# Kernel optimization log

Measured on AMD Instinct MI355X. Metric: run time of the kernel, lower is better.

Reference implementation:

```python
import jax, jax.numpy as jnp
import numpy as np

LOG_VAR_Q = 0.0
TEMPERATURE = 0.5


def setup_inputs() -> dict:
    key = jax.random.key(0)
    k1, k2, k3 = jax.random.split(key, 3)
    bs, dim_z, W, H, K = 64, 64, 32, 32, 1024
    x = jax.random.normal(k1, (bs, dim_z, W, H), dtype=jnp.float32)
    codebook = jax.random.normal(k2, (K, dim_z), dtype=jnp.float32)
    log_var_q_scalar = jnp.asarray(0.0, dtype=jnp.float32)
    # pre-sampled standard Gumbel noise for the relaxed categorical
    u = jax.random.uniform(k3, (bs * W * H, K), dtype=jnp.float32,
                           minval=1e-6, maxval=1.0 - 1e-6)
    gumbel_noise = -jnp.log(-jnp.log(u))
    return {"x": x, "codebook": codebook,
            "log_var_q_scalar": log_var_q_scalar,
            "gumbel_noise": gumbel_noise}


def reference(x, codebook, log_var_q_scalar, gumbel_noise):
    bs, dim_z, W, H = x.shape
    # [bs, dim_z, W, H] -> [bs*W*H, dim_z]
    x_flat = jnp.transpose(x, (0, 2, 3, 1)).reshape(-1, dim_z)

    var_q = jnp.exp(jnp.asarray(LOG_VAR_Q, x.dtype)) + jnp.exp(log_var_q_scalar)
    precision_q = 1.0 / jnp.clip(var_q, 1e-10)
    w = 0.5 * precision_q  # scalar weight on squared distances

    sq_x = jnp.sum(x_flat * x_flat, axis=-1, keepdims=True)
    sq_c = jnp.sum(codebook * codebook, axis=-1)
    cross = jnp.einsum('nd,kd->nk', x_flat, codebook)
    logit = -w * (sq_x - 2.0 * cross + sq_c)

    log_probs = jax.nn.log_softmax(logit, axis=-1)
    probs = jnp.exp(log_probs)

    # gumbel-softmax relaxed one-hot encodings
    encodings = jax.nn.softmax((logit + gumbel_noise) / TEMPERATURE, axis=-1)

    quantized = jnp.einsum('nk,kd->nd', encodings, codebook)
    quantized = jnp.transpose(quantized.reshape(bs, W, H, dim_z), (0, 3, 1, 2))

    kld_discrete = jnp.sum(probs * log_probs) / bs
    kld_continuous = jnp.mean(jnp.sum(w * (x - quantized) ** 2, axis=(1, 2, 3)))
    return quantized, kld_discrete + kld_continuous
```

## Files before the change

kernel.cpp:

```cpp
#include <hip/hip_runtime.h>
#include <math.h>

#define K_CB 1024
#define D_Z  64
#define MT   32
#define NTOT 65536
#define NBLK (NTOT / MT)

typedef __attribute__((ext_vector_type(8)))  short s16x8;
typedef __attribute__((ext_vector_type(4)))  short s16x4;
typedef __attribute__((ext_vector_type(4)))  float f32x4;
typedef __attribute__((ext_vector_type(16))) float f32x16;

#define WS_CB16  0
#define WS_CBT16 131072
#define WS_NWSQC 262144
#define WS_PART  266240

__device__ __forceinline__ unsigned short f2b(float f) {
  unsigned int u = __float_as_uint(f);
  u += 0x7fffu + ((u >> 16) & 1u);
  return (unsigned short)(u >> 16);
}

__global__ void vq_prep(const float* __restrict__ cb, const float* __restrict__ lvq,
                        unsigned char* __restrict__ wsb) {
  unsigned short* cb16  = (unsigned short*)(wsb + WS_CB16);
  unsigned short* cbT16 = (unsigned short*)(wsb + WS_CBT16);
  float* nwsqc = (float*)(wsb + WS_NWSQC);
  const float w = 0.5f / fmaxf(1.0f + __expf(lvq[0]), 1e-10f);
  const int tid = threadIdx.x;
  const int k  = blockIdx.x * 16 + (tid >> 4);
  const int d0 = (tid & 15) * 4;
  const f32x4 v = *(const f32x4*)(cb + k * D_Z + d0);
  s16x4 b4;
  #pragma unroll
  for (int i = 0; i < 4; i++) b4[i] = (short)f2b(v[i]);
  *(s16x4*)(cb16 + k * D_Z + d0) = b4;
  #pragma unroll
  for (int i = 0; i < 4; i++) cbT16[(d0 + i) * K_CB + k] = (unsigned short)b4[i];
  float s = v[0]*v[0] + v[1]*v[1] + v[2]*v[2] + v[3]*v[3];
  #pragma unroll
  for (int off = 1; off < 16; off <<= 1) s += __shfl_xor(s, off);
  if ((tid & 15) == 0) nwsqc[k] = -w * s;
}

__global__ __launch_bounds__(512, 4)
void vq_main(const float* __restrict__ x, const float* __restrict__ gum,
             const float* __restrict__ lvq, unsigned char* __restrict__ wsb,
             float* __restrict__ out) {
  __shared__ __align__(16) unsigned short xa[MT * D_Z];
  __shared__ __align__(16) unsigned short es[MT * K_CB];
  __shared__ __align__(16) float stats[8][MT][4];
  __shared__ __align__(16) float s2s[8][MT];
  __shared__ float kldrow[MT];
  __shared__ float wred[8];

  const int tid  = threadIdx.x;
  const int w    = tid >> 6;
  const int lane = tid & 63;
  const int m32  = lane & 31;
  const int hi   = lane >> 5;
  const int bid  = blockIdx.x;
  const int blk  = ((bid & 7) << 8) | (bid >> 3);
  const int row0 = blk * MT;
  const int bidx = row0 >> 10;
  const int rem0 = row0 & 1023;
  const int kw0  = w << 7;

  const float wq = 0.5f / fmaxf(1.0f + __expf(lvq[0]), 1e-10f);
  const float w2 = 2.0f * wq;

  const unsigned short* cb16  = (const unsigned short*)(wsb + WS_CB16);
  const unsigned short* cbT16 = (const unsigned short*)(wsb + WS_CBT16);
  const float* nwsqc = (const float*)(wsb + WS_NWSQC);

  {
    const int m = tid & 31, dg = tid >> 5;
    #pragma unroll
    for (int i = 0; i < 4; i++) {
      const int d = dg + 16 * i;
      const float v = x[((bidx * D_Z + d) << 10) + rem0 + m];
      xa[(m * D_Z + d) ^ ((m & 7) << 3)] = f2b(v);
    }
  }
  __syncthreads();

  f32x16 acc[4];
  #pragma unroll
  for (int t = 0; t < 4; t++)
    #pragma unroll
    for (int r = 0; r < 16; r++) acc[t][r] = 0.f;
  {
    s16x8 bx[4];
    #pragma unroll
    for (int kb = 0; kb < 4; kb++) {
      const int byteoff = (m32 * 128 + kb * 32 + hi * 16) ^ ((m32 & 7) << 4);
      bx[kb] = *(const s16x8*)((const unsigned char*)xa + byteoff);
    }
    #pragma unroll
    for (int t = 0; t < 4; t++) {
      const unsigned short* ap = cb16 + (kw0 + t * 32 + m32) * D_Z + hi * 8;
      #pragma unroll
      for (int kb = 0; kb < 4; kb++) {
        const s16x8 a = *(const s16x8*)(ap + kb * 16);
        acc[t] = __builtin_amdgcn_mfma_f32_32x32x16_bf16(a, bx[kb], acc[t], 0, 0, 0);
      }
    }
  }

  float m1 = -3.4e38f;
  #pragma unroll
  for (int t = 0; t < 4; t++) {
    #pragma unroll
    for (int q = 0; q < 4; q++) {
      const f32x4 nw = *(const f32x4*)(nwsqc + kw0 + t * 32 + q * 8 + hi * 4);
      #pragma unroll
      for (int i = 0; i < 4; i++) {
        acc[t][q * 4 + i] = fmaf(w2, acc[t][q * 4 + i], nw[i]);
        m1 = fmaxf(m1, acc[t][q * 4 + i]);
      }
    }
  }
  m1 = fmaxf(m1, __shfl_xor(m1, 32));

  const float* gp = gum + ((size_t)(row0 + m32) << 10) + kw0 + hi * 4;
  f32x4 gA[8];
  #pragma unroll
  for (int u = 0; u < 8; u++)
    gA[u] = *(const f32x4*)(gp + (u >> 2) * 32 + (u & 3) * 8);

  float s1 = 0.f, Aa = 0.f;
  #pragma unroll
  for (int t = 0; t < 4; t++) {
    #pragma unroll
    for (int r = 0; r < 16; r++) {
      const float u = acc[t][r] - m1;
      const float e = __expf(u);
      s1 += e;
      Aa = fmaf(u, e, Aa);
    }
  }
  s1 += __shfl_xor(s1, 32);
  Aa += __shfl_xor(Aa, 32);

  float m2 = -3.4e38f;
  #pragma unroll
  for (int u = 0; u < 8; u++) {
    const int t = u >> 2, q = u & 3;
    #pragma unroll
    for (int i = 0; i < 4; i++) {
      const float z = 2.0f * (acc[t][q * 4 + i] + gA[u][i]);
      acc[t][q * 4 + i] = z;
      m2 = fmaxf(m2, z);
    }
  }
  f32x4 gB[8];
  #pragma unroll
  for (int u = 0; u < 8; u++)
    gB[u] = *(const f32x4*)(gp + 64 + (u >> 2) * 32 + (u & 3) * 8);
  #pragma unroll
  for (int u = 0; u < 8; u++) {
    const int t = 2 + (u >> 2), q = u & 3;
    #pragma unroll
    for (int i = 0; i < 4; i++) {
      const float z = 2.0f * (acc[t][q * 4 + i] + gB[u][i]);
      acc[t][q * 4 + i] = z;
      m2 = fmaxf(m2, z);
    }
  }
  m2 = fmaxf(m2, __shfl_xor(m2, 32));
  if (hi == 0) {
    f32x4 st = {m1, s1, Aa, m2};
    *(f32x4*)&stats[w][m32][0] = st;
  }
  __syncthreads();

  float M2 = -3.4e38f;
  {
    f32x4 st[8];
    #pragma unroll
    for (int q = 0; q < 8; q++) {
      st[q] = *(const f32x4*)&stats[q][m32][0];
      M2 = fmaxf(M2, st[q][3]);
    }
    if (w == 0) {
      float M1 = -3.4e38f;
      #pragma unroll
      for (int q = 0; q < 8; q++) M1 = fmaxf(M1, st[q][0]);
      float s1g = 0.f, Ag = 0.f;
      #pragma unroll
      for (int q = 0; q < 8; q++) {
        const float dm = st[q][0] - M1;
        const float c  = __expf(dm);
        s1g += c * st[q][1];
        Ag = fmaf(c, fmaf(dm, st[q][1], st[q][2]), Ag);
      }
      if (hi == 0) kldrow[m32] = Ag / s1g - __logf(s1g);
    }
  }

  float s2 = 0.f;
  #pragma unroll
  for (int t = 0; t < 4; t++) {
    #pragma unroll
    for (int q = 0; q < 4; q++) {
      float e[4];
      #pragma unroll
      for (int i = 0; i < 4; i++) {
        e[i] = __expf(acc[t][q * 4 + i] - M2);
        s2 += e[i];
      }
      const unsigned int p0 = (unsigned int)f2b(e[0]) | ((unsigned int)f2b(e[1]) << 16);
      const unsigned int p1 = (unsigned int)f2b(e[2]) | ((unsigned int)f2b(e[3]) << 16);
      const unsigned long long pk = (unsigned long long)p0 | ((unsigned long long)p1 << 32);
      const int byteoff = (m32 * 2048 + (kw0 + t * 32 + q * 8 + hi * 4) * 2) ^ ((m32 & 7) << 4);
      *(unsigned long long*)((unsigned char*)es + byteoff) = pk;
    }
  }
  s2 += __shfl_xor(s2, 32);
  if (hi == 0) s2s[w][m32] = s2;
  __syncthreads();

  const int m16 = lane & 15, g = lane >> 4;
  const int db = w >> 1, mb = w & 1;
  const int mrow = mb * 16 + m16;
  float s2g = 0.f;
  #pragma unroll
  for (int q = 0; q < 8; q++) s2g += s2s[q][mrow];
  const float inv2 = 1.0f / s2g;

  f32x4 qacc = (f32x4){0.f, 0.f, 0.f, 0.f};
  {
    const unsigned short* a2p = cbT16 + (db * 16 + m16) * K_CB + g * 8;
    const unsigned char* esb = (const unsigned char*)es;
    #pragma unroll
    for (int kc = 0; kc < 32; kc++) {
      const s16x8 a2 = *(const s16x8*)(a2p + kc * 32);
      const int byteoff = (mrow * 2048 + kc * 64 + g * 16) ^ ((m16 & 7) << 4);
      const s16x8 b2 = *(const s16x8*)(esb + byteoff);
      qacc = __builtin_amdgcn_mfma_f32_16x16x32_bf16(a2, b2, qacc, 0, 0, 0);
    }
  }

  float kca = 0.f;
  #pragma unroll
  for (int r = 0; r < 4; r++) {
    const int d = db * 16 + g * 4 + r;
    const int off = ((bidx * D_Z + d) << 10) + rem0 + mrow;
    const float qv = qacc[r] * inv2;
    const float xv = x[off];
    out[off] = qv;
    const float dx = xv - qv;
    kca = fmaf(dx, dx, kca);
  }
  #pragma unroll
  for (int off = 1; off < 64; off <<= 1) kca += __shfl_xor(kca, off);
  if (lane == 0) wred[w] = kca;
  __syncthreads();
  if (tid == 0) {
    float tot = 0.f;
    #pragma unroll
    for (int q = 0; q < 8; q++) tot += wred[q];
    tot *= wq;
    #pragma unroll
    for (int i = 0; i < MT; i++) tot += kldrow[i];
    ((float*)(wsb + WS_PART))[blk] = tot;
  }
}

__global__ void vq_reduce(const unsigned char* __restrict__ wsb, float* __restrict__ out) {
  __shared__ float red[256];
  const float* part = (const float*)(wsb + WS_PART);
  const int t = threadIdx.x;
  float s = 0.f;
  for (int i = t; i < NBLK; i += 256) s += part[i];
  red[t] = s;
  __syncthreads();
  for (int st = 128; st > 0; st >>= 1) {
    if (t < st) red[t] += red[t + st];
    __syncthreads();
  }
  if (t == 0) out[NTOT * D_Z] = red[0] * (1.0f / 64.0f);
}

extern "C" void kernel_launch(void* const* d_in, const int* in_sizes, int n_in,
                              void* d_out, int out_size, void* d_ws, size_t ws_size,
                              hipStream_t stream) {
  const float* x   = (const float*)d_in[0];
  const float* cb  = (const float*)d_in[1];
  const float* lvq = (const float*)d_in[2];
  const float* gum = (const float*)d_in[3];
  float* out = (float*)d_out;
  unsigned char* wsb = (unsigned char*)d_ws;

  hipLaunchKernelGGL(vq_prep,   dim3(64),   dim3(256), 0, stream, cb, lvq, wsb);
  hipLaunchKernelGGL(vq_main,   dim3(NBLK), dim3(512), 0, stream, x, gum, lvq, wsb, out);
  hipLaunchKernelGGL(vq_reduce, dim3(1),    dim3(256), 0, stream, wsb, out);
}
```

Baseline: 160.5 us.

## Use packed bf16 conversion, set MFMA priority, relax launch bounds, reuse LDS x

Replaces the manual float-to-bf16 rounding with HIP intrinsics, including a packed two-value conversion for the softmax weights written to LDS. It raises wave priority around both MFMA loops and lowers the launch-bounds occupancy hint from 4 to 2, giving the compiler more registers per thread. The final KL term now reads x from the bf16 copy already in shared memory instead of reloading fp32 x from global memory. That makes the continuous KL term use bf16-rounded x, which slightly changes the loss value.

```diff
diff --git a/kernel.cpp b/kernel.cpp
--- a/kernel.cpp
+++ b/kernel.cpp
@@ -1,4 +1,5 @@
 #include <hip/hip_runtime.h>
+#include <hip/hip_bf16.h>
 #include <math.h>
 
 #define K_CB 1024
@@ -18,9 +19,16 @@
 #define WS_PART  266240
 
 __device__ __forceinline__ unsigned short f2b(float f) {
-  unsigned int u = __float_as_uint(f);
-  u += 0x7fffu + ((u >> 16) & 1u);
-  return (unsigned short)(u >> 16);
+  __hip_bfloat16 h = __float2bfloat16(f);
+  return *(unsigned short*)&h;
+}
+__device__ __forceinline__ unsigned int pk2b(float lo, float hi) {
+  float2 v; v.x = lo; v.y = hi;
+  __hip_bfloat162 h = __float22bfloat162_rn(v);
+  return *(unsigned int*)&h;
+}
+__device__ __forceinline__ float b2f(unsigned short u) {
+  return __uint_as_float(((unsigned int)u) << 16);
 }
 
 __global__ void vq_prep(const float* __restrict__ cb, const float* __restrict__ lvq,
@@ -45,7 +53,7 @@
   if ((tid & 15) == 0) nwsqc[k] = -w * s;
 }
 
-__global__ __launch_bounds__(512, 4)
+__global__ __launch_bounds__(512, 2)
 void vq_main(const float* __restrict__ x, const float* __restrict__ gum,
              const float* __restrict__ lvq, unsigned char* __restrict__ wsb,
              float* __restrict__ out) {
@@ -98,6 +106,7 @@
       const int byteoff = (m32 * 128 + kb * 32 + hi * 16) ^ ((m32 & 7) << 4);
       bx[kb] = *(const s16x8*)((const unsigned char*)xa + byteoff);
     }
+    __builtin_amdgcn_s_setprio(1);
     #pragma unroll
     for (int t = 0; t < 4; t++) {
       const unsigned short* ap = cb16 + (kw0 + t * 32 + m32) * D_Z + hi * 8;
@@ -107,6 +116,7 @@
         acc[t] = __builtin_amdgcn_mfma_f32_32x32x16_bf16(a, bx[kb], acc[t], 0, 0, 0);
       }
     }
+    __builtin_amdgcn_s_setprio(0);
   }
 
   float m1 = -3.4e38f;
@@ -211,8 +221,8 @@
         e[i] = __expf(acc[t][q * 4 + i] - M2);
         s2 += e[i];
       }
-      const unsigned int p0 = (unsigned int)f2b(e[0]) | ((unsigned int)f2b(e[1]) << 16);
-      const unsigned int p1 = (unsigned int)f2b(e[2]) | ((unsigned int)f2b(e[3]) << 16);
+      const unsigned int p0 = pk2b(e[0], e[1]);
+      const unsigned int p1 = pk2b(e[2], e[3]);
       const unsigned long long pk = (unsigned long long)p0 | ((unsigned long long)p1 << 32);
       const int byteoff = (m32 * 2048 + (kw0 + t * 32 + q * 8 + hi * 4) * 2) ^ ((m32 & 7) << 4);
       *(unsigned long long*)((unsigned char*)es + byteoff) = pk;
@@ -222,7 +232,7 @@
   if (hi == 0) s2s[w][m32] = s2;
   __syncthreads();
 
-  const int m16 = lane & 15, g = lane >> 4;
+  const int m16 = lane & 15, g16 = lane >> 4;
   const int db = w >> 1, mb = w & 1;
   const int mrow = mb * 16 + m16;
   float s2g = 0.f;
@@ -232,27 +242,32 @@
 
   f32x4 qacc = (f32x4){0.f, 0.f, 0.f, 0.f};
   {
-    const unsigned short* a2p = cbT16 + (db * 16 + m16) * K_CB + g * 8;
+    const unsigned short* a2p = cbT16 + (db * 16 + m16) * K_CB + g16 * 8;
     const unsigned char* esb = (const unsigned char*)es;
+    __builtin_amdgcn_s_setprio(1);
     #pragma unroll
     for (int kc = 0; kc < 32; kc++) {
       const s16x8 a2 = *(const s16x8*)(a2p + kc * 32);
-      const int byteoff = (mrow * 2048 + kc * 64 + g * 16) ^ ((m16 & 7) << 4);
+      const int byteoff = (mrow * 2048 + kc * 64 + g16 * 16) ^ ((m16 & 7) << 4);
       const s16x8 b2 = *(const s16x8*)(esb + byteoff);
       qacc = __builtin_amdgcn_mfma_f32_16x16x32_bf16(a2, b2, qacc, 0, 0, 0);
     }
+    __builtin_amdgcn_s_setprio(0);
   }
 
   float kca = 0.f;
-  #pragma unroll
-  for (int r = 0; r < 4; r++) {
-    const int d = db * 16 + g * 4 + r;
-    const int off = ((bidx * D_Z + d) << 10) + rem0 + mrow;
-    const float qv = qacc[r] * inv2;
-    const float xv = x[off];
-    out[off] = qv;
-    const float dx = xv - qv;
-    kca = fmaf(dx, dx, kca);
+  {
+    const int d0 = db * 16 + g16 * 4;
+    const s16x4 xb = *(const s16x4*)&xa[(mrow * D_Z + d0) ^ ((mrow & 7) << 3)];
+    #pragma unroll
+    for (int r = 0; r < 4; r++) {
+      const int d = d0 + r;
+      const int off = ((bidx * D_Z + d) << 10) + rem0 + mrow;
+      const float qv = qacc[r] * inv2;
+      out[off] = qv;
+      const float dx = b2f((unsigned short)xb[r]) - qv;
+      kca = fmaf(dx, dx, kca);
+    }
   }
   #pragma unroll
   for (int off = 1; off < 64; off <<= 1) kca += __shfl_xor(kca, off);
```

Result: slower. 197.9 us (+23.4%).
